# Kernel tuning notes

Hardware: AMD Instinct MI355X
Metric: run time of the kernel (lower is better)

Reference implementation:

```python
import jax, jax.numpy as jnp
import numpy as np
from jax import lax

TEMPERATURE = 0.5
MOMENTUM = 0.9
EPS = 1e-12  # F.normalize eps

B, D, K = 8192, 512, 16384


def _l2norm(x):
    # matches F.normalize(p=2): x / max(||x||, eps)
    n = jnp.sqrt(jnp.sum(x * x, axis=-1, keepdims=True))
    return x / jnp.maximum(n, EPS)


def setup_inputs() -> dict:
    key = jax.random.key(0)
    k1, k2, k3 = jax.random.split(key, 3)
    embeddings = jax.random.normal(k1, (B, D), dtype=jnp.float32)
    cluster_ids = jax.random.randint(k2, (B,), 0, K, dtype=jnp.int64)
    prototypes = jax.random.normal(k3, (K, D), dtype=jnp.float32)
    return {"embeddings": embeddings, "cluster_ids": cluster_ids, "prototypes": prototypes}


def reference(embeddings, cluster_ids, prototypes):
    emb_n = _l2norm(embeddings)            # [B, D]
    proto_n = _l2norm(prototypes)          # [K, D]
    sim = jnp.einsum('bd,kd->bk', emb_n, proto_n) / TEMPERATURE  # [B, K]

    pos = jnp.take_along_axis(sim, cluster_ids[:, None], axis=1)  # [B, 1]
    # mask out the positive column, then stable logsumexp over negatives
    is_pos = jnp.arange(sim.shape[1])[None, :] == cluster_ids[:, None]  # [B, K]
    neg = jnp.where(is_pos, -jnp.inf, sim)
    lse = jax.scipy.special.logsumexp(neg, axis=1, keepdims=True)       # [B, 1]
    loss = jnp.mean(-pos + lse)

    # serial momentum EMA update (order-dependent for duplicate cluster ids)
    def step(protos, xc):
        x, c = xc
        row = MOMENTUM * protos[c] + (1.0 - MOMENTUM) * x
        return protos.at[c].set(row), None

    new_protos, _ = lax.scan(step, prototypes, (embeddings, cluster_ids))
    return loss, new_protos
```

## Files before the change

kernel.cpp:

```cpp
#include <hip/hip_runtime.h>
#include <hip/hip_bf16.h>


#define B_N 8192
#define D_N 512
#define K_N 16384
#define INV_T 2.0f
#define MOM 0.9f

#define BM 128
#define BN 128
#define BKF 128
#define SPLIT 32
#define TILES ((K_N / SPLIT) / BN)
#define CHUNKS (D_N / BKF)
#define CAP 64

typedef __attribute__((ext_vector_type(8))) int intx8;
typedef __attribute__((ext_vector_type(4))) float floatx4;

__device__ __forceinline__ void gl_lds16(const void* g, void* lds) {
    __builtin_amdgcn_global_load_lds(
        (const __attribute__((address_space(1))) void*)g,
        (__attribute__((address_space(3))) void*)lds, 16, 0, 0);
}

__global__ void norm_kernel(const float* __restrict__ emb, const float* __restrict__ pro,
                            unsigned char* __restrict__ embq, unsigned char* __restrict__ proq,
                            float* __restrict__ rowsum, float* __restrict__ out) {
    if (blockIdx.x < 32) rowsum[blockIdx.x * 256 + threadIdx.x] = 0.0f;
    if (blockIdx.x == 32 && threadIdx.x == 0) out[0] = 0.0f;
    int row = blockIdx.x * 4 + (threadIdx.x >> 6);
    int lane = threadIdx.x & 63;
    const float* x;
    unsigned char* o;
    if (row < B_N) {
        x = emb + (size_t)row * D_N;
        o = embq + (size_t)row * D_N;
    } else {
        x = pro + (size_t)(row - B_N) * D_N;
        o = proq + (size_t)(row - B_N) * D_N;
    }
    const float4* xp = (const float4*)(x + lane * 8);
    float4 v0 = xp[0];
    float4 v1 = xp[1];
    float ss = v0.x * v0.x + v0.y * v0.y + v0.z * v0.z + v0.w * v0.w +
               v1.x * v1.x + v1.y * v1.y + v1.z * v1.z + v1.w * v1.w;
    #pragma unroll
    for (int of = 32; of; of >>= 1) ss += __shfl_xor(ss, of);
    float sc = 16.0f / fmaxf(sqrtf(ss), 1e-12f);
    int w0 = 0, w1 = 0;
    w0 = __builtin_amdgcn_cvt_pk_fp8_f32(v0.x * sc, v0.y * sc, w0, false);
    w0 = __builtin_amdgcn_cvt_pk_fp8_f32(v0.z * sc, v0.w * sc, w0, true);
    w1 = __builtin_amdgcn_cvt_pk_fp8_f32(v1.x * sc, v1.y * sc, w1, false);
    w1 = __builtin_amdgcn_cvt_pk_fp8_f32(v1.z * sc, v1.w * sc, w1, true);
    int2 st = {w0, w1};
    *(int2*)(o + lane * 8) = st;
}

__global__ void pos_kernel(const float* __restrict__ emb, const float* __restrict__ pro,
                           const int* __restrict__ cid, float* __restrict__ rowpos) {
    int b = blockIdx.x * 4 + (threadIdx.x >> 6);
    int lane = threadIdx.x & 63;
    int c = cid[b];
    const float4* ep = (const float4*)(emb + (size_t)b * D_N + lane * 8);
    const float4* pp = (const float4*)(pro + (size_t)c * D_N + lane * 8);
    float4 e0 = ep[0], e1 = ep[1], p0 = pp[0], p1 = pp[1];
    float dp = e0.x * p0.x + e0.y * p0.y + e0.z * p0.z + e0.w * p0.w +
               e1.x * p1.x + e1.y * p1.y + e1.z * p1.z + e1.w * p1.w;
    float ee = e0.x * e0.x + e0.y * e0.y + e0.z * e0.z + e0.w * e0.w +
               e1.x * e1.x + e1.y * e1.y + e1.z * e1.z + e1.w * e1.w;
    float qq = p0.x * p0.x + p0.y * p0.y + p0.z * p0.z + p0.w * p0.w +
               p1.x * p1.x + p1.y * p1.y + p1.z * p1.z + p1.w * p1.w;
    #pragma unroll
    for (int o = 32; o; o >>= 1) {
        dp += __shfl_xor(dp, o);
        ee += __shfl_xor(ee, o);
        qq += __shfl_xor(qq, o);
    }
    if (lane == 0)
        rowpos[b] = INV_T * dp / (fmaxf(sqrtf(ee), 1e-12f) * fmaxf(sqrtf(qq), 1e-12f));
}

__global__ __launch_bounds__(256) void flash_kernel(const unsigned char* __restrict__ embq,
                                                    const unsigned char* __restrict__ proq,
                                                    float* __restrict__ rowsum_g) {
    __shared__ __align__(16) unsigned char As[BM * BKF];
    __shared__ __align__(16) unsigned char Bs[BN * BKF];
    const int t = threadIdx.x;
    const int w = t >> 6, lane = t & 63;
    const int quad = lane >> 4, lcol = lane & 15;
    const int wm = w >> 1, wn = w & 1;
    const int rowBase = blockIdx.x * BM;
    const int nBegin = blockIdx.y * (K_N / SPLIT);

    const int fsw0 = (((quad << 1) | 0) ^ (lcol & 7)) << 4;
    const int fsw1 = (((quad << 1) | 1) ^ (lcol & 7)) << 4;
    const unsigned char* aF = &As[(wm * 64 + lcol) * BKF];
    const unsigned char* bF = &Bs[(wn * 64 + lcol) * BKF];
    const int srow = w * 8 + (lane >> 3);
    const int scol = ((lane & 7) ^ (lane >> 3)) << 4;
    const unsigned char* aS = embq + (size_t)(rowBase + srow) * D_N + scol;
    const unsigned char* bS = proq + (size_t)(nBegin + srow) * D_N + scol;

    float rowsum[16];
    #pragma unroll
    for (int i = 0; i < 16; i++) rowsum[i] = 0.0f;

    #pragma unroll
    for (int p = 0; p < 4; p++) {
        gl_lds16(aS + p * 32 * D_N, &As[p * 4096 + w * 1024]);
        gl_lds16(bS + p * 32 * D_N, &Bs[p * 4096 + w * 1024]);
    }

    for (int tile = 0; tile < TILES; tile++) {
        floatx4 acc[4][4];
        #pragma unroll
        for (int mt = 0; mt < 4; mt++)
            #pragma unroll
            for (int nt = 0; nt < 4; nt++) {
                floatx4 z = {0.0f, 0.0f, 0.0f, 0.0f};
                acc[mt][nt] = z;
            }
        #pragma unroll
        for (int ch = 0; ch < CHUNKS; ch++) {
            __syncthreads();
            intx8 af[4], bf[4];
            #pragma unroll
            for (int mt = 0; mt < 4; mt++) {
                int4 lo = *(const int4*)(aF + mt * 16 * BKF + fsw0);
                int4 hi = *(const int4*)(aF + mt * 16 * BKF + fsw1);
                intx8 v = {lo.x, lo.y, lo.z, lo.w, hi.x, hi.y, hi.z, hi.w};
                af[mt] = v;
            }
            #pragma unroll
            for (int nt = 0; nt < 4; nt++) {
                int4 lo = *(const int4*)(bF + nt * 16 * BKF + fsw0);
                int4 hi = *(const int4*)(bF + nt * 16 * BKF + fsw1);
                intx8 v = {lo.x, lo.y, lo.z, lo.w, hi.x, hi.y, hi.z, hi.w};
                bf[nt] = v;
            }
            __syncthreads();
            if (ch + 1 < CHUNKS) {
                #pragma unroll
                for (int p = 0; p < 4; p++) {
                    gl_lds16(aS + p * 32 * D_N + (ch + 1) * BKF, &As[p * 4096 + w * 1024]);
                    gl_lds16(bS + p * 32 * D_N + (ch + 1) * BKF, &Bs[p * 4096 + w * 1024]);
                }
            } else if (tile + 1 < TILES) {
                #pragma unroll
                for (int p = 0; p < 4; p++) {
                    gl_lds16(aS + p * 32 * D_N, &As[p * 4096 + w * 1024]);
                    gl_lds16(bS + (size_t)BN * D_N + p * 32 * D_N, &Bs[p * 4096 + w * 1024]);
                }
            }
            #pragma unroll
            for (int mt = 0; mt < 4; mt++)
                #pragma unroll
                for (int nt = 0; nt < 4; nt++)
                    acc[mt][nt] = __builtin_amdgcn_mfma_scale_f32_16x16x128_f8f6f4(
                        af[mt], bf[nt], acc[mt][nt], 0, 0, 0, 0x7F7F7F7F, 0, 0x7F7F7F7F);
        }
        bS += (size_t)BN * D_N;
        #pragma unroll
        for (int mt = 0; mt < 4; mt++)
            #pragma unroll
            for (int nt = 0; nt < 4; nt++)
                #pragma unroll
                for (int r = 0; r < 4; r++)
                    rowsum[mt * 4 + r] += __expf(acc[mt][nt][r] * (INV_T / 256.0f));
    }
    #pragma unroll
    for (int i = 0; i < 16; i++) {
        #pragma unroll
        for (int o = 1; o < 16; o <<= 1) rowsum[i] += __shfl_xor(rowsum[i], o);
    }
    if (lcol == 0) {
        #pragma unroll
        for (int mt = 0; mt < 4; mt++)
            #pragma unroll
            for (int r = 0; r < 4; r++)
                atomicAdd(&rowsum_g[rowBase + wm * 64 + mt * 16 + quad * 4 + r],
                          rowsum[mt * 4 + r]);
    }
}

__global__ void loss_kernel(const float* __restrict__ rowsum, const float* __restrict__ rowpos,
                            float* __restrict__ out, int* __restrict__ cnt) {
    __shared__ float red[256];
    int t = threadIdx.x;
    int b = blockIdx.x * 256 + t;
    cnt[b * 2] = 0;
    cnt[b * 2 + 1] = 0;
    float p = rowpos[b];
    red[t] = logf(rowsum[b] - __expf(p)) - p;
    __syncthreads();
    for (int o = 128; o; o >>= 1) {
        if (t < o) red[t] += red[t + o];
        __syncthreads();
    }
    if (t == 0) atomicAdd(out, red[0] * (1.0f / (float)B_N));
}

__global__ void ema_count(const int* __restrict__ cid, int* __restrict__ cnt,
                          int* __restrict__ bucket) {
    int b = blockIdx.x * 256 + threadIdx.x;
    int c = cid[b];
    int slot = atomicAdd(&cnt[c], 1);
    if (slot < CAP) bucket[c * CAP + slot] = b;
}

__global__ void ema_apply(const float* __restrict__ emb, const float* __restrict__ pro,
                          const int* __restrict__ cnt, const int* __restrict__ bucket,
                          float* __restrict__ outp) {
    int k = blockIdx.x * 4 + (threadIdx.x >> 6);
    int lane = threadIdx.x & 63;
    int n = cnt[k];
    n = n < CAP ? n : CAP;
    const float4* pp = (const float4*)(pro + (size_t)k * D_N + lane * 8);
    float4 a0 = pp[0], a1 = pp[1];
    int myb = (lane < n) ? bucket[k * CAP + lane] : 0x7fffffff;
    for (int i = 0; i < n; i++) {
        int m = myb;
        #pragma unroll
        for (int o = 1; o < 64; o <<= 1) {
            int v = __shfl_xor(m, o);
            m = v < m ? v : m;
        }
        const float4* ep = (const float4*)(emb + (size_t)m * D_N + lane * 8);
        float4 e0 = ep[0], e1 = ep[1];
        a0.x = MOM * a0.x + (1.0f - MOM) * e0.x;
        a0.y = MOM * a0.y + (1.0f - MOM) * e0.y;
        a0.z = MOM * a0.z + (1.0f - MOM) * e0.z;
        a0.w = MOM * a0.w + (1.0f - MOM) * e0.w;
        a1.x = MOM * a1.x + (1.0f - MOM) * e1.x;
        a1.y = MOM * a1.y + (1.0f - MOM) * e1.y;
        a1.z = MOM * a1.z + (1.0f - MOM) * e1.z;
        a1.w = MOM * a1.w + (1.0f - MOM) * e1.w;
        if (myb == m) myb = 0x7fffffff;
    }
    float4* op = (float4*)(outp + (size_t)k * D_N + lane * 8);
    op[0] = a0;
    op[1] = a1;
}

extern "C" void kernel_launch(void* const* d_in, const int* in_sizes, int n_in,
                              void* d_out, int out_size, void* d_ws, size_t ws_size,
                              hipStream_t stream) {
    const float* emb = (const float*)d_in[0];
    const int* cid = (const int*)d_in[1];
    const float* pro = (const float*)d_in[2];
    float* out = (float*)d_out;

    char* ws = (char*)d_ws;
    unsigned char* embq = (unsigned char*)ws;
    unsigned char* proq = (unsigned char*)(ws + 4194304);
    float* rowsum = (float*)(ws + 12582912);
    float* rowpos = (float*)(ws + 12615680);
    int* cnt = (int*)(ws + 4194304);
    int* bucket = (int*)(ws + 4194304 + 65536);

    norm_kernel<<<(B_N + K_N) / 4, 256, 0, stream>>>(emb, pro, embq, proq, rowsum, out);
    pos_kernel<<<B_N / 4, 256, 0, stream>>>(emb, pro, cid, rowpos);
    flash_kernel<<<dim3(B_N / BM, SPLIT), 256, 0, stream>>>(embq, proq, rowsum);
    loss_kernel<<<B_N / 256, 256, 0, stream>>>(rowsum, rowpos, out, cnt);
    ema_count<<<B_N / 256, 256, 0, stream>>>(cid, cnt, bucket);
    ema_apply<<<K_N / 4, 256, 0, stream>>>(emb, pro, cnt, bucket, out + 1);
}
```

Measured before the change: 204.5 us.

## Switch flash GEMM to 32x32x64 FP8 MFMA and merge norm/pos kernels

The flash kernel now uses the 32x32x64 scaled FP8 MFMA on 2x2 tiles per wave in place of 4x4 tiles of 16x16x128. The LDS layout and swizzle change to split each 128-byte K-chunk into two 64-byte halves, and the epilogue reduction and row indexing are updated to match. The norm and positive-logit kernels are fused into a single head kernel, and the count buffer is moved so it can be zeroed early, letting ema_count run before the flash kernel. The aim is fewer LDS fragment reads per MFMA, better MFMA throughput and fewer launches, at the cost of more accumulator registers and a more complex index mapping.

```diff
diff --git a/kernel.cpp b/kernel.cpp
--- a/kernel.cpp
+++ b/kernel.cpp
@@ -10,14 +10,13 @@
 
 #define BM 128
 #define BN 128
-#define BKF 128
 #define SPLIT 32
 #define TILES ((K_N / SPLIT) / BN)
-#define CHUNKS (D_N / BKF)
+#define CHUNKS (D_N / 128)
 #define CAP 64
 
 typedef __attribute__((ext_vector_type(8))) int intx8;
-typedef __attribute__((ext_vector_type(4))) float floatx4;
+typedef __attribute__((ext_vector_type(16))) float floatx16;
 
 __device__ __forceinline__ void gl_lds16(const void* g, void* lds) {
     __builtin_amdgcn_global_load_lds(
@@ -25,173 +24,192 @@
         (__attribute__((address_space(3))) void*)lds, 16, 0, 0);
 }
 
-__global__ void norm_kernel(const float* __restrict__ emb, const float* __restrict__ pro,
+__global__ void head_kernel(const float* __restrict__ emb, const float* __restrict__ pro,
+                            const int* __restrict__ cid,
                             unsigned char* __restrict__ embq, unsigned char* __restrict__ proq,
-                            float* __restrict__ rowsum, float* __restrict__ out) {
-    if (blockIdx.x < 32) rowsum[blockIdx.x * 256 + threadIdx.x] = 0.0f;
-    if (blockIdx.x == 32 && threadIdx.x == 0) out[0] = 0.0f;
-    int row = blockIdx.x * 4 + (threadIdx.x >> 6);
-    int lane = threadIdx.x & 63;
-    const float* x;
-    unsigned char* o;
-    if (row < B_N) {
-        x = emb + (size_t)row * D_N;
-        o = embq + (size_t)row * D_N;
+                            float* __restrict__ rowpos, float* __restrict__ rowsum,
+                            float* __restrict__ out, int* __restrict__ cnt) {
+    int bx = blockIdx.x;
+    int t = threadIdx.x;
+    int lane = t & 63;
+    if (bx < (B_N + K_N) / 4) {
+        if (bx < 32) rowsum[bx * 256 + t] = 0.0f;
+        if (bx == 32 && t == 0) out[0] = 0.0f;
+        int row = bx * 4 + (t >> 6);
+        const float* x;
+        unsigned char* o;
+        if (row < B_N) {
+            x = emb + (size_t)row * D_N;
+            o = embq + (size_t)row * D_N;
+        } else {
+            x = pro + (size_t)(row - B_N) * D_N;
+            o = proq + (size_t)(row - B_N) * D_N;
+        }
+        const float4* xp = (const float4*)(x + lane * 8);
+        float4 v0 = xp[0];
+        float4 v1 = xp[1];
+        float ss = v0.x * v0.x + v0.y * v0.y + v0.z * v0.z + v0.w * v0.w +
+                   v1.x * v1.x + v1.y * v1.y + v1.z * v1.z + v1.w * v1.w;
+        #pragma unroll
+        for (int of = 32; of; of >>= 1) ss += __shfl_xor(ss, of);
+        float sc = 16.0f / fmaxf(sqrtf(ss), 1e-12f);
+        int w0 = 0, w1 = 0;
+        w0 = __builtin_amdgcn_cvt_pk_fp8_f32(v0.x * sc, v0.y * sc, w0, false);
+        w0 = __builtin_amdgcn_cvt_pk_fp8_f32(v0.z * sc, v0.w * sc, w0, true);
+        w1 = __builtin_amdgcn_cvt_pk_fp8_f32(v1.x * sc, v1.y * sc, w1, false);
+        w1 = __builtin_amdgcn_cvt_pk_fp8_f32(v1.z * sc, v1.w * sc, w1, true);
+        int2 st = {w0, w1};
+        *(int2*)(o + lane * 8) = st;
     } else {
-        x = pro + (size_t)(row - B_N) * D_N;
-        o = proq + (size_t)(row - B_N) * D_N;
-    }
-    const float4* xp = (const float4*)(x + lane * 8);
-    float4 v0 = xp[0];
-    float4 v1 = xp[1];
-    float ss = v0.x * v0.x + v0.y * v0.y + v0.z * v0.z + v0.w * v0.w +
-               v1.x * v1.x + v1.y * v1.y + v1.z * v1.z + v1.w * v1.w;
-    #pragma unroll
-    for (int of = 32; of; of >>= 1) ss += __shfl_xor(ss, of);
-    float sc = 16.0f / fmaxf(sqrtf(ss), 1e-12f);
-    int w0 = 0, w1 = 0;
-    w0 = __builtin_amdgcn_cvt_pk_fp8_f32(v0.x * sc, v0.y * sc, w0, false);
-    w0 = __builtin_amdgcn_cvt_pk_fp8_f32(v0.z * sc, v0.w * sc, w0, true);
-    w1 = __builtin_amdgcn_cvt_pk_fp8_f32(v1.x * sc, v1.y * sc, w1, false);
-    w1 = __builtin_amdgcn_cvt_pk_fp8_f32(v1.z * sc, v1.w * sc, w1, true);
-    int2 st = {w0, w1};
-    *(int2*)(o + lane * 8) = st;
-}
-
-__global__ void pos_kernel(const float* __restrict__ emb, const float* __restrict__ pro,
-                           const int* __restrict__ cid, float* __restrict__ rowpos) {
-    int b = blockIdx.x * 4 + (threadIdx.x >> 6);
-    int lane = threadIdx.x & 63;
-    int c = cid[b];
-    const float4* ep = (const float4*)(emb + (size_t)b * D_N + lane * 8);
-    const float4* pp = (const float4*)(pro + (size_t)c * D_N + lane * 8);
-    float4 e0 = ep[0], e1 = ep[1], p0 = pp[0], p1 = pp[1];
-    float dp = e0.x * p0.x + e0.y * p0.y + e0.z * p0.z + e0.w * p0.w +
-               e1.x * p1.x + e1.y * p1.y + e1.z * p1.z + e1.w * p1.w;
-    float ee = e0.x * e0.x + e0.y * e0.y + e0.z * e0.z + e0.w * e0.w +
-               e1.x * e1.x + e1.y * e1.y + e1.z * e1.z + e1.w * e1.w;
-    float qq = p0.x * p0.x + p0.y * p0.y + p0.z * p0.z + p0.w * p0.w +
-               p1.x * p1.x + p1.y * p1.y + p1.z * p1.z + p1.w * p1.w;
-    #pragma unroll
-    for (int o = 32; o; o >>= 1) {
-        dp += __shfl_xor(dp, o);
-        ee += __shfl_xor(ee, o);
-        qq += __shfl_xor(qq, o);
-    }
-    if (lane == 0)
-        rowpos[b] = INV_T * dp / (fmaxf(sqrtf(ee), 1e-12f) * fmaxf(sqrtf(qq), 1e-12f));
+        int pb = bx - (B_N + K_N) / 4;
+        if (t < 8) cnt[pb * 8 + t] = 0;
+        int b = pb * 4 + (t >> 6);
+        int c = cid[b];
+        const float4* ep = (const float4*)(emb + (size_t)b * D_N + lane * 8);
+        const float4* pp = (const float4*)(pro + (size_t)c * D_N + lane * 8);
+        float4 e0 = ep[0], e1 = ep[1], p0 = pp[0], p1 = pp[1];
+        float dp = e0.x * p0.x + e0.y * p0.y + e0.z * p0.z + e0.w * p0.w +
+                   e1.x * p1.x + e1.y * p1.y + e1.z * p1.z + e1.w * p1.w;
+        float ee = e0.x * e0.x + e0.y * e0.y + e0.z * e0.z + e0.w * e0.w +
+                   e1.x * e1.x + e1.y * e1.y + e1.z * e1.z + e1.w * e1.w;
+        float qq = p0.x * p0.x + p0.y * p0.y + p0.z * p0.z + p0.w * p0.w +
+                   p1.x * p1.x + p1.y * p1.y + p1.z * p1.z + p1.w * p1.w;
+        #pragma unroll
+        for (int o = 32; o; o >>= 1) {
+            dp += __shfl_xor(dp, o);
+            ee += __shfl_xor(ee, o);
+            qq += __shfl_xor(qq, o);
+        }
+        if (lane == 0)
+            rowpos[b] = INV_T * dp / (fmaxf(sqrtf(ee), 1e-12f) * fmaxf(sqrtf(qq), 1e-12f));
+    }
 }
 
 __global__ __launch_bounds__(256) void flash_kernel(const unsigned char* __restrict__ embq,
                                                     const unsigned char* __restrict__ proq,
                                                     float* __restrict__ rowsum_g) {
-    __shared__ __align__(16) unsigned char As[BM * BKF];
-    __shared__ __align__(16) unsigned char Bs[BN * BKF];
+    __shared__ __align__(16) unsigned char As[BM * 128];
+    __shared__ __align__(16) unsigned char Bs[BN * 128];
     const int t = threadIdx.x;
     const int w = t >> 6, lane = t & 63;
-    const int quad = lane >> 4, lcol = lane & 15;
+    const int m = lane & 31, q2 = lane >> 5;
     const int wm = w >> 1, wn = w & 1;
     const int rowBase = blockIdx.x * BM;
     const int nBegin = blockIdx.y * (K_N / SPLIT);
 
-    const int fsw0 = (((quad << 1) | 0) ^ (lcol & 7)) << 4;
-    const int fsw1 = (((quad << 1) | 1) ^ (lcol & 7)) << 4;
-    const unsigned char* aF = &As[(wm * 64 + lcol) * BKF];
-    const unsigned char* bF = &Bs[(wn * 64 + lcol) * BKF];
-    const int srow = w * 8 + (lane >> 3);
-    const int scol = ((lane & 7) ^ (lane >> 3)) << 4;
-    const unsigned char* aS = embq + (size_t)(rowBase + srow) * D_N + scol;
-    const unsigned char* bS = proq + (size_t)(nBegin + srow) * D_N + scol;
-
-    float rowsum[16];
-    #pragma unroll
-    for (int i = 0; i < 16; i++) rowsum[i] = 0.0f;
-
+    const int e = (m >> 1) & 3;
+    const int s0 = (((q2 << 1) | 0) ^ e) << 4;
+    const int s1 = s0 ^ 16;
+    const unsigned char* aR = &As[(wm * 64 + m) * 64];
+    const unsigned char* bR = &Bs[(wn * 64 + m) * 64];
+
+    const unsigned char* aSrcP[4];
+    const unsigned char* bSrcP[4];
     #pragma unroll
     for (int p = 0; p < 4; p++) {
-        gl_lds16(aS + p * 32 * D_N, &As[p * 4096 + w * 1024]);
-        gl_lds16(bS + p * 32 * D_N, &Bs[p * 4096 + w * 1024]);
+        int f = p * 256 + t;
+        int r = (f >> 2) & 127;
+        int h = f >> 9;
+        int g = (f & 3) ^ ((r >> 1) & 3);
+        aSrcP[p] = embq + (size_t)(rowBase + r) * D_N + h * 64 + g * 16;
+        bSrcP[p] = proq + (size_t)(nBegin + r) * D_N + h * 64 + g * 16;
+    }
+
+    float rowsum[32];
+    #pragma unroll
+    for (int i = 0; i < 32; i++) rowsum[i] = 0.0f;
+
+    #pragma unroll
+    for (int p = 0; p < 4; p++) {
+        gl_lds16(aSrcP[p], &As[p * 4096 + w * 1024]);
+        gl_lds16(bSrcP[p], &Bs[p * 4096 + w * 1024]);
     }
 
     for (int tile = 0; tile < TILES; tile++) {
-        floatx4 acc[4][4];
-        #pragma unroll
-        for (int mt = 0; mt < 4; mt++)
-            #pragma unroll
-            for (int nt = 0; nt < 4; nt++) {
-                floatx4 z = {0.0f, 0.0f, 0.0f, 0.0f};
-                acc[mt][nt] = z;
-            }
+        floatx16 acc[2][2];
+        #pragma unroll
+        for (int mt = 0; mt < 2; mt++)
+            #pragma unroll
+            for (int nt = 0; nt < 2; nt++)
+                #pragma unroll
+                for (int r = 0; r < 16; r++) acc[mt][nt][r] = 0.0f;
         #pragma unroll
         for (int ch = 0; ch < CHUNKS; ch++) {
             __syncthreads();
-            intx8 af[4], bf[4];
-            #pragma unroll
-            for (int mt = 0; mt < 4; mt++) {
-                int4 lo = *(const int4*)(aF + mt * 16 * BKF + fsw0);
-                int4 hi = *(const int4*)(aF + mt * 16 * BKF + fsw1);
-                intx8 v = {lo.x, lo.y, lo.z, lo.w, hi.x, hi.y, hi.z, hi.w};
-                af[mt] = v;
-            }
-            #pragma unroll
-            for (int nt = 0; nt < 4; nt++) {
-                int4 lo = *(const int4*)(bF + nt * 16 * BKF + fsw0);
-                int4 hi = *(const int4*)(bF + nt * 16 * BKF + fsw1);
-                intx8 v = {lo.x, lo.y, lo.z, lo.w, hi.x, hi.y, hi.z, hi.w};
-                bf[nt] = v;
-            }
+            intx8 af[2][2], bf[2][2];
+            #pragma unroll
+            for (int mt = 0; mt < 2; mt++)
+                #pragma unroll
+                for (int h = 0; h < 2; h++) {
+                    int4 lo = *(const int4*)(aR + mt * 2048 + h * 8192 + s0);
+                    int4 hi = *(const int4*)(aR + mt * 2048 + h * 8192 + s1);
+                    intx8 v = {lo.x, lo.y, lo.z, lo.w, hi.x, hi.y, hi.z, hi.w};
+                    af[mt][h] = v;
+                }
+            #pragma unroll
+            for (int nt = 0; nt < 2; nt++)
+                #pragma unroll
+                for (int h = 0; h < 2; h++) {
+                    int4 lo = *(const int4*)(bR + nt * 2048 + h * 8192 + s0);
+                    int4 hi = *(const int4*)(bR + nt * 2048 + h * 8192 + s1);
+                    intx8 v = {lo.x, lo.y, lo.z, lo.w, hi.x, hi.y, hi.z, hi.w};
+                    bf[nt][h] = v;
+                }
             __syncthreads();
             if (ch + 1 < CHUNKS) {
                 #pragma unroll
                 for (int p = 0; p < 4; p++) {
-                    gl_lds16(aS + p * 32 * D_N + (ch + 1) * BKF, &As[p * 4096 + w * 1024]);
-                    gl_lds16(bS + p * 32 * D_N + (ch + 1) * BKF, &Bs[p * 4096 + w * 1024]);
+                    gl_lds16(aSrcP[p] + (ch + 1) * 128, &As[p * 4096 + w * 1024]);
+                    gl_lds16(bSrcP[p] + (ch + 1) * 128, &Bs[p * 4096 + w * 1024]);
                 }
             } else if (tile + 1 < TILES) {
                 #pragma unroll
                 for (int p = 0; p < 4; p++) {
-                    gl_lds16(aS + p * 32 * D_N, &As[p * 4096 + w * 1024]);
-                    gl_lds16(bS + (size_t)BN * D_N + p * 32 * D_N, &Bs[p * 4096 + w * 1024]);
+                    gl_lds16(aSrcP[p], &As[p * 4096 + w * 1024]);
+                    gl_lds16(bSrcP[p] + (size_t)BN * D_N, &Bs[p * 4096 + w * 1024]);
                 }
             }
             #pragma unroll
-            for (int mt = 0; mt < 4; mt++)
-                #pragma unroll
-                for (int nt = 0; nt < 4; nt++)
-                    acc[mt][nt] = __builtin_amdgcn_mfma_scale_f32_16x16x128_f8f6f4(
-                        af[mt], bf[nt], acc[mt][nt], 0, 0, 0, 0x7F7F7F7F, 0, 0x7F7F7F7F);
-        }
-        bS += (size_t)BN * D_N;
-        #pragma unroll
-        for (int mt = 0; mt < 4; mt++)
-            #pragma unroll
-            for (int nt = 0; nt < 4; nt++)
-                #pragma unroll
-                for (int r = 0; r < 4; r++)
-                    rowsum[mt * 4 + r] += __expf(acc[mt][nt][r] * (INV_T / 256.0f));
-    }
-    #pragma unroll
-    for (int i = 0; i < 16; i++) {
-        #pragma unroll
-        for (int o = 1; o < 16; o <<= 1) rowsum[i] += __shfl_xor(rowsum[i], o);
-    }
-    if (lcol == 0) {
-        #pragma unroll
-        for (int mt = 0; mt < 4; mt++)
-            #pragma unroll
-            for (int r = 0; r < 4; r++)
-                atomicAdd(&rowsum_g[rowBase + wm * 64 + mt * 16 + quad * 4 + r],
-                          rowsum[mt * 4 + r]);
+            for (int mt = 0; mt < 2; mt++)
+                #pragma unroll
+                for (int nt = 0; nt < 2; nt++)
+                    #pragma unroll
+                    for (int h = 0; h < 2; h++)
+                        acc[mt][nt] = __builtin_amdgcn_mfma_scale_f32_32x32x64_f8f6f4(
+                            af[mt][h], bf[nt][h], acc[mt][nt], 0, 0, 0, 0x7F7F7F7F, 0,
+                            0x7F7F7F7F);
+        }
+        #pragma unroll
+        for (int p = 0; p < 4; p++) bSrcP[p] += (size_t)BN * D_N;
+        #pragma unroll
+        for (int mt = 0; mt < 2; mt++)
+            #pragma unroll
+            for (int nt = 0; nt < 2; nt++)
+                #pragma unroll
+                for (int r = 0; r < 16; r++)
+                    rowsum[mt * 16 + r] += __expf(acc[mt][nt][r] * (INV_T / 256.0f));
+    }
+    #pragma unroll
+    for (int i = 0; i < 32; i++) {
+        #pragma unroll
+        for (int o = 1; o < 32; o <<= 1) rowsum[i] += __shfl_xor(rowsum[i], o);
+    }
+    if (m == 0) {
+        #pragma unroll
+        for (int mt = 0; mt < 2; mt++)
+            #pragma unroll
+            for (int r = 0; r < 16; r++)
+                atomicAdd(&rowsum_g[rowBase + wm * 64 + mt * 32 + (r & 3) + 8 * (r >> 2) +
+                                    4 * q2],
+                          rowsum[mt * 16 + r]);
     }
 }
 
 __global__ void loss_kernel(const float* __restrict__ rowsum, const float* __restrict__ rowpos,
-                            float* __restrict__ out, int* __restrict__ cnt) {
+                            float* __restrict__ out) {
     __shared__ float red[256];
     int t = threadIdx.x;
     int b = blockIdx.x * 256 + t;
-    cnt[b * 2] = 0;
-    cnt[b * 2 + 1] = 0;
     float p = rowpos[b];
     red[t] = logf(rowsum[b] - __expf(p)) - p;
     __syncthreads();
@@ -257,13 +275,13 @@
     unsigned char* proq = (unsigned char*)(ws + 4194304);
     float* rowsum = (float*)(ws + 12582912);
     float* rowpos = (float*)(ws + 12615680);
-    int* cnt = (int*)(ws + 4194304);
-    int* bucket = (int*)(ws + 4194304 + 65536);
-
-    norm_kernel<<<(B_N + K_N) / 4, 256, 0, stream>>>(emb, pro, embq, proq, rowsum, out);
-    pos_kernel<<<B_N / 4, 256, 0, stream>>>(emb, pro, cid, rowpos);
+    int* cnt = (int*)(ws + 12648448);
+    int* bucket = (int*)(ws + 12713984);
+
+    head_kernel<<<(B_N + K_N) / 4 + B_N / 4, 256, 0, stream>>>(emb, pro, cid, embq, proq,
+                                                               rowpos, rowsum, out, cnt);
+    ema_count<<<B_N / 256, 256, 0, stream>>>(cid, cnt, bucket);
     flash_kernel<<<dim3(B_N / BM, SPLIT), 256, 0, stream>>>(embq, proq, rowsum);
-    loss_kernel<<<B_N / 256, 256, 0, stream>>>(rowsum, rowpos, out, cnt);
-    ema_count<<<B_N / 256, 256, 0, stream>>>(cid, cnt, bucket);
+    loss_kernel<<<B_N / 256, 256, 0, stream>>>(rowsum, rowpos, out);
     ema_apply<<<K_N / 4, 256, 0, stream>>>(emb, pro, cnt, bucket, out + 1);
 }
```

Result: slower. 214.6 us (+4.9%).
